# Kernel tuning notes

Hardware: AMD Instinct MI355X
Metric: run time of the kernel (lower is better)

The kernel has to match this reference:

```python
import jax, jax.numpy as jnp
import numpy as np

DIM = 384; HEADS = 6; K = 10; G = 2
GC = DIM // G            # group channel dim
HD = DIM // HEADS        # head dim
SCALE = HD ** -0.5
LN_EPS = 1e-5


def _sqdist(a, b):
    # a: [..., n, 3], b: [..., m, 3] -> [..., n, m]
    return (jnp.sum(a * a, -1)[..., :, None]
            + jnp.sum(b * b, -1)[..., None, :]
            - 2.0 * jnp.einsum('...nc,...mc->...nm', a, b))


def setup_inputs() -> dict:
    key = jax.random.key(0)
    ks = jax.random.split(key, 12)
    B, N, M = 4, 1024, 1024
    s = 0.02
    return {
        'q': jax.random.normal(ks[0], (B, N, DIM), jnp.float32),
        'q_pos': jax.random.normal(ks[1], (B, N, 3), jnp.float32),
        'v': jax.random.normal(ks[2], (B, M, DIM), jnp.float32),
        'v_pos': jax.random.normal(ks[3], (B, M, 3), jnp.float32),
        'Wq': jax.random.normal(ks[4], (DIM, DIM), jnp.float32) * s,
        'Wk': jax.random.normal(ks[5], (DIM, DIM), jnp.float32) * s,
        'Wv': jax.random.normal(ks[6], (DIM, DIM), jnp.float32) * s,
        'Wvoff': jax.random.normal(ks[7], (DIM, DIM), jnp.float32) * s,
        'Woff1': jax.random.normal(ks[8], (DIM, 2 * GC), jnp.float32) * s,
        'boff1': jnp.zeros((DIM,), jnp.float32),
        'ln_g': jnp.ones((DIM,), jnp.float32),
        'ln_b': jnp.zeros((DIM,), jnp.float32),
        'Woff2': jax.random.normal(ks[9], (3, DIM), jnp.float32) * s,
        'Wproj': jax.random.normal(ks[10], (DIM, DIM), jnp.float32) * s,
        'bproj': jnp.zeros((DIM,), jnp.float32),
    }


def reference(q, q_pos, v, v_pos, Wq, Wk, Wv, Wvoff, Woff1, boff1,
              ln_g, ln_b, Woff2, Wproj, bproj):
    B, N, C = q.shape
    M = v.shape[1]

    # --- knn_point: K nearest v_pos for each q_pos ---
    idx = jax.lax.top_k(-_sqdist(q_pos, v_pos), K)[1]        # [B,N,K]
    idx_flat = idx.reshape(B, N * K, 1)

    qp = q @ Wq.T                                            # [B,N,C]
    v_off = v @ Wvoff.T                                      # [B,M,C]

    # index_points gathers
    local_v = jnp.take_along_axis(v_off, idx_flat, axis=1).reshape(B, N, K, C)
    local_v_pos = jnp.take_along_axis(v_pos, idx_flat, axis=1).reshape(B, N, K, 3)

    # group split: 'b n k (g c) -> b g n k c'
    off_local_v = local_v.reshape(B, N, K, G, GC).transpose(0, 3, 1, 2, 4)  # [B,G,N,K,GC]
    group_q = qp.reshape(B, N, G, GC).transpose(0, 2, 1, 3)                 # [B,G,N,GC]

    shift_feat = jnp.concatenate(
        [off_local_v, jnp.broadcast_to(group_q[:, :, :, None, :], (B, G, N, K, GC))], -1)

    # linear_offset MLP: Linear -> LayerNorm -> GELU(exact) -> Linear, then tanh
    h = shift_feat @ Woff1.T + boff1                          # [B,G,N,K,DIM]
    mu = h.mean(-1, keepdims=True)
    var = h.var(-1, keepdims=True)
    h = (h - mu) / jnp.sqrt(var + LN_EPS) * ln_g + ln_b
    h = jax.nn.gelu(h, approximate=False)
    offset = jnp.tanh(h @ Woff2.T)                            # [B,G,N,K,3]

    shift_pos = (local_v_pos[:, None] + offset).reshape(B, G, N * K, 3)
    vg = v.reshape(B, M, G, GC).transpose(0, 2, 1, 3)         # [B,G,M,GC]

    # --- three_nn + reciprocal-distance three_interpolate ---
    sqd = _sqdist(shift_pos, v_pos[:, None])                  # [B,G,N*K,M]
    negd, idx3 = jax.lax.top_k(-sqd, 3)                       # 3 smallest
    dist = jnp.sqrt(jnp.maximum(-negd, 0.0))                  # [B,G,N*K,3]
    w = 1.0 / (dist + 1e-8)
    w = w / jnp.sum(w, -1, keepdims=True)
    feats = jnp.take_along_axis(vg, idx3.reshape(B, G, N * K * 3, 1), axis=2)
    feats = feats.reshape(B, G, N * K, 3, GC)
    interp = jnp.einsum('bgnj,bgnjc->bgnc', w, feats)         # [B,G,N*K,GC]
    # '(b g) (n k) c -> b n k (g c)'
    interp = interp.reshape(B, G, N, K, GC).transpose(0, 2, 3, 1, 4).reshape(B, N, K, C)

    # --- local cross-attention (each query attends to its K interpolated feats) ---
    kf = (interp @ Wk.T).reshape(B, N, K, HEADS, HD)
    vf = (interp @ Wv.T).reshape(B, N, K, HEADS, HD)
    qh = qp.reshape(B, N, HEADS, HD)
    attn = jnp.einsum('bnhd,bnkhd->bhnk', qh, kf) * SCALE
    attn = jax.nn.softmax(attn, axis=-1)
    out = jnp.einsum('bhnk,bnkhd->bnhd', attn, vf).reshape(B, N, C)
    return out @ Wproj.T + bproj
```

## Files before the change

### kernel.cpp

```cpp
#include <hip/hip_runtime.h>
#include <math.h>

#define NB 4
#define NN 1024
#define NM 1024
#define NC 384
#define NK 10
#define NG 2
#define NGC 192
#define NH 6

#define GSZ ((size_t)NB * NM * NC)
#define QSZ ((size_t)NB * NN * NC)
#define NCNC ((size_t)NC * NC)

#define OFF_WQ 0
#define OFF_W1B 147456
#define OFF_WK0 221184
#define OFF_WK1 294912
#define OFF_WV0 368640
#define OFF_WV1 442368
#define OFF_WPROJ 516096
#define WT_ALL_FLOATS 663552

__device__ __forceinline__ float wred_sum(float v) {
#pragma unroll
  for (int m = 32; m >= 1; m >>= 1) v += __shfl_xor(v, m, 64);
  return v;
}

__device__ __forceinline__ void wred_argmin(float& d, int& m) {
#pragma unroll
  for (int off = 32; off >= 1; off >>= 1) {
    float od = __shfl_xor(d, off, 64);
    int om = __shfl_xor(m, off, 64);
    if (od < d || (od == d && om < m)) { d = od; m = om; }
  }
}

__device__ __forceinline__ ushort f2bf(float x) {
  unsigned u = __float_as_uint(x);
  unsigned r = (u + 0x7fffu + ((u >> 16) & 1u)) >> 16;
  return (ushort)r;
}
__device__ __forceinline__ float b2f(ushort s) {
  return __uint_as_float(((unsigned)s) << 16);
}

__global__ void transpose_all_k(const float* __restrict__ Wq, const float* __restrict__ Woff1,
                                const float* __restrict__ Wk, const float* __restrict__ Wv,
                                const float* __restrict__ Wproj, float* __restrict__ Wt_all) {
  const float* W;
  int i0, icount, doff;
  switch (blockIdx.y) {
    case 0: W = Wq;    i0 = 0;   icount = NC;  doff = OFF_WQ;    break;
    case 1: W = Woff1; i0 = NGC; icount = NGC; doff = OFF_W1B;   break;
    case 2: W = Wk;    i0 = 0;   icount = NGC; doff = OFF_WK0;   break;
    case 3: W = Wk;    i0 = NGC; icount = NGC; doff = OFF_WK1;   break;
    case 4: W = Wv;    i0 = 0;   icount = NGC; doff = OFF_WV0;   break;
    case 5: W = Wv;    i0 = NGC; icount = NGC; doff = OFF_WV1;   break;
    default: W = Wproj; i0 = 0;  icount = NC;  doff = OFF_WPROJ; break;
  }
  int id = blockIdx.x * 256 + threadIdx.x;
  if (id >= icount * NC) return;
  int o = id % NC;
  int i = id / NC;
  Wt_all[doff + (size_t)i * NC + o] = W[(size_t)o * NC + i0 + i];
}

__global__ void wcomb_k(const float* __restrict__ Woff1, const float* __restrict__ Wvoff,
                        float* __restrict__ Wcomb_t) {
  int o = blockIdx.x;
  int g = blockIdx.y;
  int i = threadIdx.x;
  __shared__ float w1[NGC];
  if (i < NGC) w1[i] = Woff1[(size_t)o * NC + i];
  __syncthreads();
  float acc = 0.f;
#pragma unroll 4
  for (int j = 0; j < NGC; ++j)
    acc = fmaf(w1[j], Wvoff[(size_t)(g * NGC + j) * NC + i], acc);
  Wcomb_t[((size_t)g * NC + i) * NC + o] = acc;
}

__global__ __launch_bounds__(384) void gemm16_k(const float* __restrict__ X, int IN, int xoff0,
                                                int xoff_stride, const float* __restrict__ Wt0,
                                                size_t wstride, const float* __restrict__ bias,
                                                float* __restrict__ Y0, size_t ystride) {
  __shared__ __align__(16) float xs[NC][20];
  int tid = threadIdx.x;
  int og = tid % 96, rg = tid / 96;
  int r0 = blockIdx.x * 16;
  int job = blockIdx.y;
  int xoff = xoff0 + job * xoff_stride;
  const float* Wt = Wt0 + (size_t)job * wstride;
  float* Y = Y0 + (size_t)job * ystride;
  for (int t = tid; t < 16 * IN; t += 384) {
    int r = t / IN, kk = t % IN;
    xs[kk][r] = X[(size_t)(r0 + r) * NC + xoff + kk];
  }
  __syncthreads();
  float acc[4][4];
#pragma unroll
  for (int i = 0; i < 4; ++i)
#pragma unroll
    for (int j = 0; j < 4; ++j) acc[i][j] = 0.f;
  int o = og * 4;
#pragma unroll 4
  for (int kk = 0; kk < IN; ++kk) {
    float4 w4 = *(const float4*)&Wt[(size_t)kk * NC + o];
    float4 x4 = *(const float4*)&xs[kk][rg * 4];
    float xr[4] = {x4.x, x4.y, x4.z, x4.w};
    float wr[4] = {w4.x, w4.y, w4.z, w4.w};
#pragma unroll
    for (int ri = 0; ri < 4; ++ri)
#pragma unroll
      for (int oi = 0; oi < 4; ++oi) acc[ri][oi] = fmaf(xr[ri], wr[oi], acc[ri][oi]);
  }
  float4 bv = make_float4(0.f, 0.f, 0.f, 0.f);
  if (bias) bv = *(const float4*)&bias[o];
#pragma unroll
  for (int ri = 0; ri < 4; ++ri) {
    float4 ov;
    ov.x = acc[ri][0] + bv.x;
    ov.y = acc[ri][1] + bv.y;
    ov.z = acc[ri][2] + bv.z;
    ov.w = acc[ri][3] + bv.w;
    *(float4*)&Y[(size_t)(r0 + rg * 4 + ri) * NC + o] = ov;
  }
}

__global__ __launch_bounds__(384) void vproj_k(const float* __restrict__ v,
                                               const float* __restrict__ Wcomb_t,
                                               const float* __restrict__ Wt_all,
                                               float* __restrict__ vcontrib,
                                               ushort* __restrict__ KcT,
                                               ushort* __restrict__ VcT) {
  __shared__ __align__(16) float xs[NC][20];
  int tid = threadIdx.x;
  int og = tid % 96, rg = tid / 96;
  int r0 = blockIdx.x * 16;
  int job = blockIdx.y;
  const float* Wt;
  float* Yf = nullptr;
  ushort* Yh = nullptr;
  int IN, xoff;
  switch (job) {
    case 0: Wt = Wcomb_t;        IN = NC;  xoff = 0;   Yf = vcontrib;       break;
    case 1: Wt = Wcomb_t + NCNC; IN = NC;  xoff = 0;   Yf = vcontrib + GSZ; break;
    case 2: Wt = Wt_all + OFF_WK0; IN = NGC; xoff = 0;   Yh = KcT;          break;
    case 3: Wt = Wt_all + OFF_WK1; IN = NGC; xoff = NGC; Yh = KcT + GSZ;    break;
    case 4: Wt = Wt_all + OFF_WV0; IN = NGC; xoff = 0;   Yh = VcT;          break;
    default: Wt = Wt_all + OFF_WV1; IN = NGC; xoff = NGC; Yh = VcT + GSZ;   break;
  }
  for (int t = tid; t < 16 * IN; t += 384) {
    int r = t / IN, kk = t % IN;
    xs[kk][r] = v[(size_t)(r0 + r) * NC + xoff + kk];
  }
  __syncthreads();
  float acc[4][4];
#pragma unroll
  for (int i = 0; i < 4; ++i)
#pragma unroll
    for (int j = 0; j < 4; ++j) acc[i][j] = 0.f;
  int o = og * 4;
#pragma unroll 4
  for (int kk = 0; kk < IN; ++kk) {
    float4 w4 = *(const float4*)&Wt[(size_t)kk * NC + o];
    float4 x4 = *(const float4*)&xs[kk][rg * 4];
    float xr[4] = {x4.x, x4.y, x4.z, x4.w};
    float wr[4] = {w4.x, w4.y, w4.z, w4.w};
#pragma unroll
    for (int ri = 0; ri < 4; ++ri)
#pragma unroll
      for (int oi = 0; oi < 4; ++oi) acc[ri][oi] = fmaf(xr[ri], wr[oi], acc[ri][oi]);
  }
  if (Yf) {
#pragma unroll
    for (int ri = 0; ri < 4; ++ri)
      *(float4*)&Yf[(size_t)(r0 + rg * 4 + ri) * NC + o] =
          make_float4(acc[ri][0], acc[ri][1], acc[ri][2], acc[ri][3]);
  } else {
#pragma unroll
    for (int ri = 0; ri < 4; ++ri) {
      ushort4 pk;
      pk.x = f2bf(acc[ri][0]);
      pk.y = f2bf(acc[ri][1]);
      pk.z = f2bf(acc[ri][2]);
      pk.w = f2bf(acc[ri][3]);
      *(ushort4*)&Yh[(size_t)(r0 + rg * 4 + ri) * NC + o] = pk;
    }
  }
}

__global__ __launch_bounds__(256) void knn2_k(const float* __restrict__ q_pos,
                                              const float* __restrict__ v_pos,
                                              int* __restrict__ knn_idx) {
  __shared__ float4 cpos[NM];
  int tid = threadIdx.x, lane = tid & 63, wid = tid >> 6;
  int b = blockIdx.x / (NN / 4);
  int n = (blockIdx.x % (NN / 4)) * 4 + wid;
  for (int t = tid; t < NM; t += 256) {
    float x = v_pos[((size_t)b * NM + t) * 3 + 0];
    float y = v_pos[((size_t)b * NM + t) * 3 + 1];
    float z = v_pos[((size_t)b * NM + t) * 3 + 2];
    cpos[t] = make_float4(x, y, z, x * x + y * y + z * z);
  }
  __syncthreads();
  float qx = q_pos[((size_t)b * NN + n) * 3 + 0];
  float qy = q_pos[((size_t)b * NN + n) * 3 + 1];
  float qz = q_pos[((size_t)b * NN + n) * 3 + 2];
  float qq = qx * qx + qy * qy + qz * qz;
  float bd[NK];
  int bi[NK];
#pragma unroll
  for (int j = 0; j < NK; ++j) { bd[j] = 1e30f; bi[j] = 0x7fffffff; }
#pragma unroll
  for (int t = 0; t < NM / 64; ++t) {
    int m = t * 64 + lane;
    float4 cc = cpos[m];
    float d = qq + cc.w - 2.f * (qx * cc.x + qy * cc.y + qz * cc.z);
    if (d < bd[NK - 1]) {
#pragma unroll
      for (int j = NK - 1; j > 0; --j) {
        if (d < bd[j - 1]) { bd[j] = bd[j - 1]; bi[j] = bi[j - 1]; }
        else if (d < bd[j]) { bd[j] = d; bi[j] = m; }
      }
      if (d < bd[0]) { bd[0] = d; bi[0] = m; }
    }
  }
  size_t base = ((size_t)b * NN + n) * NK;
#pragma unroll
  for (int round = 0; round < NK; ++round) {
    float dh = bd[0];
    int mh = bi[0];
    wred_argmin(dh, mh);
    if (lane == 0) knn_idx[base + round] = mh;
    if (bi[0] == mh) {
#pragma unroll
      for (int j = 0; j < NK - 1; ++j) { bd[j] = bd[j + 1]; bi[j] = bi[j + 1]; }
      bd[NK - 1] = 1e30f; bi[NK - 1] = 0x7fffffff;
    }
  }
}

__global__ __launch_bounds__(256) void mlp3nn_k(
    const float* __restrict__ vcontrib, const float* __restrict__ qcontrib,
    const float* __restrict__ boff1, const float* __restrict__ ln_g,
    const float* __restrict__ ln_b, const float* __restrict__ Woff2,
    const int* __restrict__ knn_idx, const float* __restrict__ v_pos,
    int* __restrict__ idx3, float* __restrict__ w3) {
  __shared__ float4 cpos[NM];
  int tid = threadIdx.x, lane = tid & 63, wid = tid >> 6;
  int r = blockIdx.x * 4 + wid;
  int b = (blockIdx.x * 4) / (NK * NN * NG);
  for (int t = tid; t < NM; t += 256) {
    float x = v_pos[((size_t)b * NM + t) * 3 + 0];
    float y = v_pos[((size_t)b * NM + t) * 3 + 1];
    float z = v_pos[((size_t)b * NM + t) * 3 + 2];
    cpos[t] = make_float4(x, y, z, x * x + y * y + z * z);
  }
  __syncthreads();
  int k = r % NK;
  int n = (r / NK) % NN;
  int g = (r / (NK * NN)) % NG;
  int m = knn_idx[((size_t)b * NN + n) * NK + k];
  const float* vc = vcontrib + ((size_t)(g * NB + b) * NM + m) * NC;
  const float* qc = qcontrib + ((size_t)(g * NB + b) * NN + n) * NC;
  float h[6];
  float s = 0.f, s2 = 0.f;
#pragma unroll
  for (int j = 0; j < 6; ++j) {
    int c = j * 64 + lane;
    float x = vc[c] + qc[c] + boff1[c];
    h[j] = x; s += x; s2 += x * x;
  }
  s = wred_sum(s);
  s2 = wred_sum(s2);
  float mean = s * (1.f / NC);
  float var = s2 * (1.f / NC) - mean * mean;
  float inv = 1.f / sqrtf(var + 1e-5f);
  float p0 = 0.f, p1 = 0.f, p2 = 0.f;
#pragma unroll
  for (int j = 0; j < 6; ++j) {
    int c = j * 64 + lane;
    float x = (h[j] - mean) * inv * ln_g[c] + ln_b[c];
    x = 0.5f * x * (1.f + erff(x * 0.70710678118654752f));
    p0 = fmaf(x, Woff2[0 * NC + c], p0);
    p1 = fmaf(x, Woff2[1 * NC + c], p1);
    p2 = fmaf(x, Woff2[2 * NC + c], p2);
  }
  p0 = wred_sum(p0);
  p1 = wred_sum(p1);
  p2 = wred_sum(p2);
  float4 cm = cpos[m];
  float sx = cm.x + tanhf(p0);
  float sy = cm.y + tanhf(p1);
  float sz = cm.z + tanhf(p2);
  float qq2 = sx * sx + sy * sy + sz * sz;
  float d0v = 1e30f, d1v = 1e30f, d2v = 1e30f;
  int i0v = 0x7fffffff, i1v = 0x7fffffff, i2v = 0x7fffffff;
#pragma unroll
  for (int t = 0; t < NM / 64; ++t) {
    int m2 = t * 64 + lane;
    float4 cc = cpos[m2];
    float d = qq2 + cc.w - 2.f * (sx * cc.x + sy * cc.y + sz * cc.z);
    if (d < d2v) {
      d2v = d; i2v = m2;
      if (d2v < d1v) { float td = d1v; d1v = d2v; d2v = td; int ti = i1v; i1v = i2v; i2v = ti; }
      if (d1v < d0v) { float td = d0v; d0v = d1v; d1v = td; int ti = i0v; i0v = i1v; i1v = ti; }
    }
  }
  float rd[3];
  int rm[3];
#pragma unroll
  for (int round = 0; round < 3; ++round) {
    float dh = d0v;
    int mh = i0v;
    wred_argmin(dh, mh);
    rd[round] = dh; rm[round] = mh;
    if (i0v == mh) {
      d0v = d1v; i0v = i1v;
      d1v = d2v; i1v = i2v;
      d2v = 1e30f; i2v = 0x7fffffff;
    }
  }
  if (lane == 0) {
    float e0 = 1.f / (sqrtf(fmaxf(rd[0], 0.f)) + 1e-8f);
    float e1 = 1.f / (sqrtf(fmaxf(rd[1], 0.f)) + 1e-8f);
    float e2 = 1.f / (sqrtf(fmaxf(rd[2], 0.f)) + 1e-8f);
    float sw = e0 + e1 + e2;
    idx3[(size_t)r * 3 + 0] = rm[0]; w3[(size_t)r * 3 + 0] = e0 / sw;
    idx3[(size_t)r * 3 + 1] = rm[1]; w3[(size_t)r * 3 + 1] = e1 / sw;
    idx3[(size_t)r * 3 + 2] = rm[2]; w3[(size_t)r * 3 + 2] = e2 / sw;
  }
}

__global__ __launch_bounds__(NC) void attn_k(const float* __restrict__ qp,
                                             const ushort* __restrict__ Kc,
                                             const ushort* __restrict__ Vc,
                                             const int* __restrict__ idx3,
                                             const float* __restrict__ w3,
                                             float* __restrict__ attn_out) {
  __shared__ int il[NG][NK][3];
  __shared__ float wl[NG][NK][3];
  int o = threadIdx.x;
  int b = blockIdx.x / NN;
  int n = blockIdx.x % NN;
  if (o < NG * NK * 3) {
    int g = o / (NK * 3), k = (o / 3) % NK, j = o % 3;
    size_t rr = (((size_t)(b * NG + g) * NN + n) * NK + k) * 3 + j;
    il[g][k][j] = idx3[rr];
    wl[g][k][j] = w3[rr];
  }
  __syncthreads();
  float qv = qp[((size_t)b * NN + n) * NC + o];
  float p[NK], vf[NK];
#pragma unroll
  for (int k = 0; k < NK; ++k) {
    float kf = 0.f, v_ = 0.f;
#pragma unroll
    for (int g = 0; g < NG; ++g)
#pragma unroll
      for (int j = 0; j < 3; ++j) {
        int m = il[g][k][j];
        float w = wl[g][k][j];
        size_t base = ((size_t)(g * NB + b) * NM + m) * NC + o;
        kf = fmaf(w, b2f(Kc[base]), kf);
        v_ = fmaf(w, b2f(Vc[base]), v_);
      }
    vf[k] = v_;
    p[k] = qv * kf;
  }
#pragma unroll
  for (int off = 32; off >= 1; off >>= 1) {
#pragma unroll
    for (int k = 0; k < NK; ++k) p[k] += __shfl_xor(p[k], off, 64);
  }
  float a[NK];
  float mx = -1e30f;
#pragma unroll
  for (int k = 0; k < NK; ++k) { a[k] = p[k] * 0.125f; mx = fmaxf(mx, a[k]); }
  float sum = 0.f;
#pragma unroll
  for (int k = 0; k < NK; ++k) { a[k] = expf(a[k] - mx); sum += a[k]; }
  float outv = 0.f;
#pragma unroll
  for (int k = 0; k < NK; ++k) outv = fmaf(a[k] / sum, vf[k], outv);
  attn_out[((size_t)b * NN + n) * NC + o] = outv;
}

extern "C" void kernel_launch(void* const* d_in, const int* in_sizes, int n_in,
                              void* d_out, int out_size, void* d_ws, size_t ws_size,
                              hipStream_t stream) {
  (void)in_sizes; (void)n_in; (void)out_size; (void)ws_size;
  const float* q     = (const float*)d_in[0];
  const float* q_pos = (const float*)d_in[1];
  const float* v     = (const float*)d_in[2];
  const float* v_pos = (const float*)d_in[3];
  const float* Wq    = (const float*)d_in[4];
  const float* Wk    = (const float*)d_in[5];
  const float* Wv    = (const float*)d_in[6];
  const float* Wvoff = (const float*)d_in[7];
  const float* Woff1 = (const float*)d_in[8];
  const float* boff1 = (const float*)d_in[9];
  const float* ln_g  = (const float*)d_in[10];
  const float* ln_b  = (const float*)d_in[11];
  const float* Woff2 = (const float*)d_in[12];
  const float* Wproj = (const float*)d_in[13];
  const float* bproj = (const float*)d_in[14];
  float* out = (float*)d_out;

  char* p = (char*)d_ws;
  auto alloc_f = [&](size_t n) { float* r = (float*)p; p += n * sizeof(float); return r; };
  auto alloc_h = [&](size_t n) { ushort* r = (ushort*)p; p += n * sizeof(ushort); return r; };
  auto alloc_i = [&](size_t n) { int* r = (int*)p; p += n * sizeof(int); return r; };

  float* qp        = alloc_f(QSZ);
  float* qcontrib  = alloc_f((size_t)NG * QSZ);
  float* vcontrib  = alloc_f((size_t)NG * GSZ);
  float* Wt_all    = alloc_f((size_t)WT_ALL_FLOATS);
  float* Wcomb_t   = alloc_f((size_t)NG * NCNC);
  float* w3        = alloc_f((size_t)NB * NG * NN * NK * 3);
  ushort* KcT      = alloc_h((size_t)NG * GSZ);
  ushort* VcT      = alloc_h((size_t)NG * GSZ);
  int* knn_idx     = alloc_i((size_t)NB * NN * NK);
  int* idx3        = alloc_i((size_t)NB * NG * NN * NK * 3);
  float* attn_out  = vcontrib;

  transpose_all_k<<<dim3(576, 7), 256, 0, stream>>>(Wq, Woff1, Wk, Wv, Wproj, Wt_all);
  wcomb_k<<<dim3(NC, NG), NC, 0, stream>>>(Woff1, Wvoff, Wcomb_t);

  gemm16_k<<<dim3(NB * NN / 16, 1), 384, 0, stream>>>(q, NC, 0, 0, Wt_all + OFF_WQ, 0, nullptr,
                                                      qp, 0);
  knn2_k<<<NB * (NN / 4), 256, 0, stream>>>(q_pos, v_pos, knn_idx);
  gemm16_k<<<dim3(NB * NN / 16, 2), 384, 0, stream>>>(qp, NGC, 0, NGC, Wt_all + OFF_W1B, 0,
                                                      nullptr, qcontrib, QSZ);
  vproj_k<<<dim3(NB * NM / 16, 6), 384, 0, stream>>>(v, Wcomb_t, Wt_all, vcontrib, KcT, VcT);

  mlp3nn_k<<<NB * NG * NN * NK / 4, 256, 0, stream>>>(vcontrib, qcontrib, boff1, ln_g, ln_b,
                                                      Woff2, knn_idx, v_pos, idx3, w3);
  attn_k<<<NB * NN, NC, 0, stream>>>(qp, KcT, VcT, idx3, w3, attn_out);
  gemm16_k<<<dim3(NB * NN / 16, 1), 384, 0, stream>>>(attn_out, NC, 0, 0, Wt_all + OFF_WPROJ, 0,
                                                      bproj, out, 0);
}
```

Before: 530.7 us.

## Process two rows per wave in mlp3nn and branchless top-3; restructure attn softmax

mlp3nn_k now has each wavefront handle two (g,n,k) rows, which halves the grid and amortizes the v_pos shared-memory load and the weight reads across two rows. The top-3 insertion in the 1024-point scan becomes a branchless fmin/fmax/select chain, with the two rows interleaved for more ILP. attn_k stages V features in shared memory and writes per-head logits through LDS, so it keeps fewer registers live instead of holding 10-element arrays. In exchange there are more registers per thread in mlp3nn, an extra barrier in attn, and fewer blocks in flight.

```diff
diff --git a/kernel.cpp b/kernel.cpp
--- a/kernel.cpp
+++ b/kernel.cpp
@@ -27,15 +27,6 @@
 #pragma unroll
   for (int m = 32; m >= 1; m >>= 1) v += __shfl_xor(v, m, 64);
   return v;
-}
-
-__device__ __forceinline__ void wred_argmin(float& d, int& m) {
-#pragma unroll
-  for (int off = 32; off >= 1; off >>= 1) {
-    float od = __shfl_xor(d, off, 64);
-    int om = __shfl_xor(m, off, 64);
-    if (od < d || (od == d && om < m)) { d = od; m = om; }
-  }
 }
 
 __device__ __forceinline__ ushort f2bf(float x) {
@@ -234,7 +225,12 @@
   for (int round = 0; round < NK; ++round) {
     float dh = bd[0];
     int mh = bi[0];
-    wred_argmin(dh, mh);
+#pragma unroll
+    for (int off = 32; off >= 1; off >>= 1) {
+      float od = __shfl_xor(dh, off, 64);
+      int om = __shfl_xor(mh, off, 64);
+      if (od < dh || (od == dh && om < mh)) { dh = od; mh = om; }
+    }
     if (lane == 0) knn_idx[base + round] = mh;
     if (bi[0] == mh) {
 #pragma unroll
@@ -252,8 +248,9 @@
     int* __restrict__ idx3, float* __restrict__ w3) {
   __shared__ float4 cpos[NM];
   int tid = threadIdx.x, lane = tid & 63, wid = tid >> 6;
-  int r = blockIdx.x * 4 + wid;
-  int b = (blockIdx.x * 4) / (NK * NN * NG);
+  int ra = blockIdx.x * 8 + wid * 2;
+  int rb = ra + 1;
+  int b = (blockIdx.x * 8) / (NK * NN * NG);
   for (int t = tid; t < NM; t += 256) {
     float x = v_pos[((size_t)b * NM + t) * 3 + 0];
     float y = v_pos[((size_t)b * NM + t) * 3 + 1];
@@ -261,78 +258,120 @@
     cpos[t] = make_float4(x, y, z, x * x + y * y + z * z);
   }
   __syncthreads();
-  int k = r % NK;
-  int n = (r / NK) % NN;
-  int g = (r / (NK * NN)) % NG;
-  int m = knn_idx[((size_t)b * NN + n) * NK + k];
-  const float* vc = vcontrib + ((size_t)(g * NB + b) * NM + m) * NC;
-  const float* qc = qcontrib + ((size_t)(g * NB + b) * NN + n) * NC;
-  float h[6];
-  float s = 0.f, s2 = 0.f;
+  int ka = ra % NK, na = (ra / NK) % NN, ga = (ra / (NK * NN)) % NG;
+  int kb = rb % NK, nb = (rb / NK) % NN, gb = (rb / (NK * NN)) % NG;
+  int ma = knn_idx[((size_t)b * NN + na) * NK + ka];
+  int mb = knn_idx[((size_t)b * NN + nb) * NK + kb];
+  const float* vca = vcontrib + ((size_t)(ga * NB + b) * NM + ma) * NC;
+  const float* qca = qcontrib + ((size_t)(ga * NB + b) * NN + na) * NC;
+  const float* vcb = vcontrib + ((size_t)(gb * NB + b) * NM + mb) * NC;
+  const float* qcb = qcontrib + ((size_t)(gb * NB + b) * NN + nb) * NC;
+  float ha[6], hb[6];
+  float sa = 0.f, s2a = 0.f, sb = 0.f, s2b = 0.f;
 #pragma unroll
   for (int j = 0; j < 6; ++j) {
     int c = j * 64 + lane;
-    float x = vc[c] + qc[c] + boff1[c];
-    h[j] = x; s += x; s2 += x * x;
-  }
-  s = wred_sum(s);
-  s2 = wred_sum(s2);
-  float mean = s * (1.f / NC);
-  float var = s2 * (1.f / NC) - mean * mean;
-  float inv = 1.f / sqrtf(var + 1e-5f);
-  float p0 = 0.f, p1 = 0.f, p2 = 0.f;
+    float bo = boff1[c];
+    float xa = vca[c] + qca[c] + bo;
+    float xb = vcb[c] + qcb[c] + bo;
+    ha[j] = xa; sa += xa; s2a += xa * xa;
+    hb[j] = xb; sb += xb; s2b += xb * xb;
+  }
+#pragma unroll
+  for (int off = 32; off >= 1; off >>= 1) {
+    sa += __shfl_xor(sa, off, 64);
+    s2a += __shfl_xor(s2a, off, 64);
+    sb += __shfl_xor(sb, off, 64);
+    s2b += __shfl_xor(s2b, off, 64);
+  }
+  float meana = sa * (1.f / NC), meanb = sb * (1.f / NC);
+  float vara = s2a * (1.f / NC) - meana * meana;
+  float varb = s2b * (1.f / NC) - meanb * meanb;
+  float inva = 1.f / sqrtf(vara + 1e-5f);
+  float invb = 1.f / sqrtf(varb + 1e-5f);
+  float p0a = 0.f, p1a = 0.f, p2a = 0.f, p0b = 0.f, p1b = 0.f, p2b = 0.f;
 #pragma unroll
   for (int j = 0; j < 6; ++j) {
     int c = j * 64 + lane;
-    float x = (h[j] - mean) * inv * ln_g[c] + ln_b[c];
-    x = 0.5f * x * (1.f + erff(x * 0.70710678118654752f));
-    p0 = fmaf(x, Woff2[0 * NC + c], p0);
-    p1 = fmaf(x, Woff2[1 * NC + c], p1);
-    p2 = fmaf(x, Woff2[2 * NC + c], p2);
-  }
-  p0 = wred_sum(p0);
-  p1 = wred_sum(p1);
-  p2 = wred_sum(p2);
-  float4 cm = cpos[m];
-  float sx = cm.x + tanhf(p0);
-  float sy = cm.y + tanhf(p1);
-  float sz = cm.z + tanhf(p2);
-  float qq2 = sx * sx + sy * sy + sz * sz;
-  float d0v = 1e30f, d1v = 1e30f, d2v = 1e30f;
-  int i0v = 0x7fffffff, i1v = 0x7fffffff, i2v = 0x7fffffff;
-#pragma unroll
+    float gg = ln_g[c], bb = ln_b[c];
+    float w0 = Woff2[0 * NC + c], w1 = Woff2[1 * NC + c], w2 = Woff2[2 * NC + c];
+    float xa = (ha[j] - meana) * inva * gg + bb;
+    xa = 0.5f * xa * (1.f + erff(xa * 0.70710678118654752f));
+    float xb = (hb[j] - meanb) * invb * gg + bb;
+    xb = 0.5f * xb * (1.f + erff(xb * 0.70710678118654752f));
+    p0a = fmaf(xa, w0, p0a); p1a = fmaf(xa, w1, p1a); p2a = fmaf(xa, w2, p2a);
+    p0b = fmaf(xb, w0, p0b); p1b = fmaf(xb, w1, p1b); p2b = fmaf(xb, w2, p2b);
+  }
+#pragma unroll
+  for (int off = 32; off >= 1; off >>= 1) {
+    p0a += __shfl_xor(p0a, off, 64);
+    p1a += __shfl_xor(p1a, off, 64);
+    p2a += __shfl_xor(p2a, off, 64);
+    p0b += __shfl_xor(p0b, off, 64);
+    p1b += __shfl_xor(p1b, off, 64);
+    p2b += __shfl_xor(p2b, off, 64);
+  }
+  float4 cma = cpos[ma], cmb = cpos[mb];
+  float sxa = cma.x + tanhf(p0a), sya = cma.y + tanhf(p1a), sza = cma.z + tanhf(p2a);
+  float sxb = cmb.x + tanhf(p0b), syb = cmb.y + tanhf(p1b), szb = cmb.z + tanhf(p2b);
+  float qqa = sxa * sxa + sya * sya + sza * sza;
+  float qqb = sxb * sxb + syb * syb + szb * szb;
+  float d0a = 1e30f, d1a = 1e30f, d2a = 1e30f;
+  float d0b = 1e30f, d1b = 1e30f, d2b = 1e30f;
+  int i0a = 0x7fffffff, i1a = 0x7fffffff, i2a = 0x7fffffff;
+  int i0b = 0x7fffffff, i1b = 0x7fffffff, i2b = 0x7fffffff;
+#pragma unroll 4
   for (int t = 0; t < NM / 64; ++t) {
     int m2 = t * 64 + lane;
     float4 cc = cpos[m2];
-    float d = qq2 + cc.w - 2.f * (sx * cc.x + sy * cc.y + sz * cc.z);
-    if (d < d2v) {
-      d2v = d; i2v = m2;
-      if (d2v < d1v) { float td = d1v; d1v = d2v; d2v = td; int ti = i1v; i1v = i2v; i2v = ti; }
-      if (d1v < d0v) { float td = d0v; d0v = d1v; d1v = td; int ti = i0v; i0v = i1v; i1v = ti; }
+    float da = qqa + cc.w - 2.f * (sxa * cc.x + sya * cc.y + sza * cc.z);
+    float db = qqb + cc.w - 2.f * (sxb * cc.x + syb * cc.y + szb * cc.z);
+    i2a = (da < d1a) ? i1a : ((da < d2a) ? m2 : i2a);
+    d2a = fminf(fmaxf(da, d1a), d2a);
+    i1a = (da < d0a) ? i0a : ((da < d1a) ? m2 : i1a);
+    d1a = fminf(fmaxf(da, d0a), d1a);
+    i0a = (da < d0a) ? m2 : i0a;
+    d0a = fminf(da, d0a);
+    i2b = (db < d1b) ? i1b : ((db < d2b) ? m2 : i2b);
+    d2b = fminf(fmaxf(db, d1b), d2b);
+    i1b = (db < d0b) ? i0b : ((db < d1b) ? m2 : i1b);
+    d1b = fminf(fmaxf(db, d0b), d1b);
+    i0b = (db < d0b) ? m2 : i0b;
+    d0b = fminf(db, d0b);
+  }
+  float rda[3], rdb[3];
+  int rma[3], rmb[3];
+#pragma unroll
+  for (int round = 0; round < 3; ++round) {
+    float dha = d0a; int mha = i0a;
+    float dhb = d0b; int mhb = i0b;
+#pragma unroll
+    for (int off = 32; off >= 1; off >>= 1) {
+      float oda = __shfl_xor(dha, off, 64); int oma = __shfl_xor(mha, off, 64);
+      float odb = __shfl_xor(dhb, off, 64); int omb = __shfl_xor(mhb, off, 64);
+      if (oda < dha || (oda == dha && oma < mha)) { dha = oda; mha = oma; }
+      if (odb < dhb || (odb == dhb && omb < mhb)) { dhb = odb; mhb = omb; }
     }
-  }
-  float rd[3];
-  int rm[3];
-#pragma unroll
-  for (int round = 0; round < 3; ++round) {
-    float dh = d0v;
-    int mh = i0v;
-    wred_argmin(dh, mh);
-    rd[round] = dh; rm[round] = mh;
-    if (i0v == mh) {
-      d0v = d1v; i0v = i1v;
-      d1v = d2v; i1v = i2v;
-      d2v = 1e30f; i2v = 0x7fffffff;
-    }
+    rda[round] = dha; rma[round] = mha;
+    rdb[round] = dhb; rmb[round] = mhb;
+    if (i0a == mha) { d0a = d1a; i0a = i1a; d1a = d2a; i1a = i2a; d2a = 1e30f; i2a = 0x7fffffff; }
+    if (i0b == mhb) { d0b = d1b; i0b = i1b; d1b = d2b; i1b = i2b; d2b = 1e30f; i2b = 0x7fffffff; }
   }
   if (lane == 0) {
-    float e0 = 1.f / (sqrtf(fmaxf(rd[0], 0.f)) + 1e-8f);
-    float e1 = 1.f / (sqrtf(fmaxf(rd[1], 0.f)) + 1e-8f);
-    float e2 = 1.f / (sqrtf(fmaxf(rd[2], 0.f)) + 1e-8f);
+    float e0 = 1.f / (sqrtf(fmaxf(rda[0], 0.f)) + 1e-8f);
+    float e1 = 1.f / (sqrtf(fmaxf(rda[1], 0.f)) + 1e-8f);
+    float e2 = 1.f / (sqrtf(fmaxf(rda[2], 0.f)) + 1e-8f);
     float sw = e0 + e1 + e2;
-    idx3[(size_t)r * 3 + 0] = rm[0]; w3[(size_t)r * 3 + 0] = e0 / sw;
-    idx3[(size_t)r * 3 + 1] = rm[1]; w3[(size_t)r * 3 + 1] = e1 / sw;
-    idx3[(size_t)r * 3 + 2] = rm[2]; w3[(size_t)r * 3 + 2] = e2 / sw;
+    idx3[(size_t)ra * 3 + 0] = rma[0]; w3[(size_t)ra * 3 + 0] = e0 / sw;
+    idx3[(size_t)ra * 3 + 1] = rma[1]; w3[(size_t)ra * 3 + 1] = e1 / sw;
+    idx3[(size_t)ra * 3 + 2] = rma[2]; w3[(size_t)ra * 3 + 2] = e2 / sw;
+    float f0 = 1.f / (sqrtf(fmaxf(rdb[0], 0.f)) + 1e-8f);
+    float f1 = 1.f / (sqrtf(fmaxf(rdb[1], 0.f)) + 1e-8f);
+    float f2 = 1.f / (sqrtf(fmaxf(rdb[2], 0.f)) + 1e-8f);
+    float sw2 = f0 + f1 + f2;
+    idx3[(size_t)rb * 3 + 0] = rmb[0]; w3[(size_t)rb * 3 + 0] = f0 / sw2;
+    idx3[(size_t)rb * 3 + 1] = rmb[1]; w3[(size_t)rb * 3 + 1] = f1 / sw2;
+    idx3[(size_t)rb * 3 + 2] = rmb[2]; w3[(size_t)rb * 3 + 2] = f2 / sw2;
   }
 }
 
@@ -342,9 +381,12 @@
                                              const int* __restrict__ idx3,
                                              const float* __restrict__ w3,
                                              float* __restrict__ attn_out) {
+  __shared__ float vfs[NK][NC];
+  __shared__ float lgs[NH][NK];
   __shared__ int il[NG][NK][3];
   __shared__ float wl[NG][NK][3];
   int o = threadIdx.x;
+  int lane = o & 63, wid = o >> 6;
   int b = blockIdx.x / NN;
   int n = blockIdx.x % NN;
   if (o < NG * NK * 3) {
@@ -355,10 +397,8 @@
   }
   __syncthreads();
   float qv = qp[((size_t)b * NN + n) * NC + o];
-  float p[NK], vf[NK];
-#pragma unroll
   for (int k = 0; k < NK; ++k) {
-    float kf = 0.f, v_ = 0.f;
+    float kf = 0.f, vf = 0.f;
 #pragma unroll
     for (int g = 0; g < NG; ++g)
 #pragma unroll
@@ -367,26 +407,23 @@
         float w = wl[g][k][j];
         size_t base = ((size_t)(g * NB + b) * NM + m) * NC + o;
         kf = fmaf(w, b2f(Kc[base]), kf);
-        v_ = fmaf(w, b2f(Vc[base]), v_);
+        vf = fmaf(w, b2f(Vc[base]), vf);
       }
-    vf[k] = v_;
-    p[k] = qv * kf;
-  }
-#pragma unroll
-  for (int off = 32; off >= 1; off >>= 1) {
-#pragma unroll
-    for (int k = 0; k < NK; ++k) p[k] += __shfl_xor(p[k], off, 64);
-  }
+    vfs[k][o] = vf;
+    float p = wred_sum(qv * kf);
+    if (lane == 0) lgs[wid][k] = p * 0.125f;
+  }
+  __syncthreads();
   float a[NK];
   float mx = -1e30f;
 #pragma unroll
-  for (int k = 0; k < NK; ++k) { a[k] = p[k] * 0.125f; mx = fmaxf(mx, a[k]); }
+  for (int k = 0; k < NK; ++k) { a[k] = lgs[wid][k]; mx = fmaxf(mx, a[k]); }
   float sum = 0.f;
 #pragma unroll
   for (int k = 0; k < NK; ++k) { a[k] = expf(a[k] - mx); sum += a[k]; }
   float outv = 0.f;
 #pragma unroll
-  for (int k = 0; k < NK; ++k) outv = fmaf(a[k] / sum, vf[k], outv);
+  for (int k = 0; k < NK; ++k) outv = fmaf(a[k] / sum, vfs[k][o], outv);
   attn_out[((size_t)b * NN + n) * NC + o] = outv;
 }
 
@@ -438,7 +475,7 @@
                                                       nullptr, qcontrib, QSZ);
   vproj_k<<<dim3(NB * NM / 16, 6), 384, 0, stream>>>(v, Wcomb_t, Wt_all, vcontrib, KcT, VcT);
 
-  mlp3nn_k<<<NB * NG * NN * NK / 4, 256, 0, stream>>>(vcontrib, qcontrib, boff1, ln_g, ln_b,
+  mlp3nn_k<<<NB * NG * NN * NK / 8, 256, 0, stream>>>(vcontrib, qcontrib, boff1, ln_g, ln_b,
                                                       Woff2, knn_idx, v_pos, idx3, w3);
   attn_k<<<NB * NN, NC, 0, stream>>>(qp, KcT, VcT, idx3, w3, attn_out);
   gemm16_k<<<dim3(NB * NN / 16, 1), 384, 0, stream>>>(attn_out, NC, 0, 0, Wt_all + OFF_WPROJ, 0,
```

Result: faster. 476.9 us (-10.1%).
